# Performance work log

Hardware: AMD Instinct MI355X
Metric: run time of the kernel (lower is better)

The kernel has to match this reference:

```python
import jax, jax.numpy as jnp
import numpy as np

B, C, COUT, HEADS = 1, 256, 256, 8
H, W, KS = 96, 96, 7  # spatial dims and neighborhood kernel size


def _nbr_1d(n, k):
    # NATTEN/flex-mask style clamped window: center = clip(q, wl, n-1-wr)
    wl = k // 2
    wr = k // 2 + (k % 2 - 1)
    q = np.arange(n)
    center = np.clip(q, wl, n - 1 - wr)
    start = center - wl  # in [0, n-k]; window always fully in-bounds
    return start[:, None] + np.arange(k)[None, :]  # [n, k]


def _nbr_idx(h, w, k):
    ih = _nbr_1d(h, k)  # [h, k]
    iw = _nbr_1d(w, k)  # [w, k]
    flat = ih[:, None, :, None] * w + iw[None, :, None, :]  # [h, w, k, k]
    return jnp.asarray(flat.reshape(h * w, k * k))  # [S, K]


def setup_inputs() -> dict:
    key = jax.random.key(0)
    ks = jax.random.split(key, 4)
    x = jax.random.normal(ks[0], (B, C, H, W), jnp.float32)
    w_qkv = jax.random.normal(ks[1], (3 * C, C), jnp.float32) * (C ** -0.5)
    b_qkv = jnp.zeros((3 * C,), jnp.float32)
    w_out = jax.random.normal(ks[2], (COUT, C), jnp.float32) * (C ** -0.5)
    b_out = jnp.zeros((COUT,), jnp.float32)
    return {"x": x, "w_qkv": w_qkv, "b_qkv": b_qkv, "w_out": w_out, "b_out": b_out}


def reference(x, w_qkv, b_qkv, w_out, b_out):
    dh = C // HEADS
    S = H * W
    xl = jnp.moveaxis(x, 1, -1)  # [B,H,W,C]
    qkv = xl @ w_qkv.T + b_qkv  # [B,H,W,3C], layout (qkv, heads, dh) on last axis
    qkv = qkv.reshape(B, S, 3, HEADS, dh)
    q = jnp.transpose(qkv[:, :, 0], (0, 2, 1, 3))  # [B,heads,S,dh]
    k = jnp.transpose(qkv[:, :, 1], (0, 2, 1, 3))
    v = jnp.transpose(qkv[:, :, 2], (0, 2, 1, 3))
    # rope_embed_fraction = 0.0 -> RoPE is identity
    nbr = _nbr_idx(H, W, KS)  # [S, K] static neighbor indices, K = KS*KS
    k_nb = jnp.take(k, nbr, axis=2)  # [B,heads,S,K,dh]
    v_nb = jnp.take(v, nbr, axis=2)  # [B,heads,S,K,dh]
    scores = jnp.einsum('bhsd,bhskd->bhsk', q, k_nb) * (dh ** -0.5)
    attn = jax.nn.softmax(scores, axis=-1)  # window fully in-bounds -> no mask
    out = jnp.einsum('bhsk,bhskd->bhsd', attn, v_nb)  # [B,heads,S,dh]
    out = jnp.transpose(out, (0, 2, 1, 3)).reshape(B, S, HEADS * dh)
    out = out @ w_out.T + b_out  # [B,S,COUT]
    out = out.reshape(B, H, W, COUT)
    return jnp.moveaxis(out, -1, 1)  # [B,COUT,H,W]
```

## Files before the change

kernel.cpp:

```cpp
#include <hip/hip_runtime.h>
#include <hip/hip_bf16.h>
#include <math.h>

#define SD 9216
#define HH 96
#define CC 256
#define NO 768
#define NH 8
#define DH 32
#define NW1 (NO * CC)
#define NWT (NW1 + CC * CC)
#define PROW 232

typedef short bf16x8 __attribute__((ext_vector_type(8)));
typedef short short8v __attribute__((ext_vector_type(8)));
typedef float f32x4 __attribute__((ext_vector_type(4)));
typedef unsigned short us8 __attribute__((ext_vector_type(8)));

__device__ __forceinline__ float bf2f(unsigned short u) {
  union { unsigned u; float f; } c; c.u = ((unsigned)u) << 16; return c.f;
}
__device__ __forceinline__ unsigned short f2bf(float f) {
  unsigned u = __float_as_uint(f);
  unsigned r = (u + 0x7FFF + ((u >> 16) & 1)) >> 16;
  return (unsigned short)r;
}
__device__ __forceinline__ void gll16(const unsigned short* g, short* l) {
  __builtin_amdgcn_global_load_lds(
      (const __attribute__((address_space(1))) void*)g,
      (__attribute__((address_space(3))) void*)l, 16, 0, 0);
}

__global__ __launch_bounds__(256) void prep(const float* __restrict__ x,
                                            const float* __restrict__ wq,
                                            const float* __restrict__ wo,
                                            unsigned short* __restrict__ xbt,
                                            unsigned short* __restrict__ wdst) {
  __shared__ float tile[32][33];
  const int b = blockIdx.x;
  const int t = threadIdx.x;
  if (b < 2304) {
    const int s0 = (b % 288) * 32;
    const int c0 = (b / 288) * 32;
    {
      const int c = t >> 3, s4 = (t & 7) * 4;
      const float4 v = *(const float4*)(x + (size_t)(c0 + c) * SD + s0 + s4);
      tile[c][s4] = v.x; tile[c][s4 + 1] = v.y; tile[c][s4 + 2] = v.z; tile[c][s4 + 3] = v.w;
    }
    __syncthreads();
    {
      const int s = t >> 3, c4 = (t & 7) * 4;
      ushort4 o;
      o.x = f2bf(tile[c4][s]);     o.y = f2bf(tile[c4 + 1][s]);
      o.z = f2bf(tile[c4 + 2][s]); o.w = f2bf(tile[c4 + 3][s]);
      *(ushort4*)(xbt + (size_t)(s0 + s) * CC + c0 + c4) = o;
    }
  } else {
    const int i = ((b - 2304) * 256 + t) * 4;
    if (i < NWT) {
      const float* src = (i < NW1) ? (wq + i) : (wo + (i - NW1));
      const float4 v = *(const float4*)src;
      ushort4 o;
      o.x = f2bf(v.x); o.y = f2bf(v.y); o.z = f2bf(v.z); o.w = f2bf(v.w);
      *(ushort4*)(wdst + i) = o;
    }
  }
}

template <int BM, int BN, int EPI>
__global__ __launch_bounds__(256) void gemm_gll(const unsigned short* __restrict__ A,
                                                const unsigned short* __restrict__ Bm,
                                                const float* __restrict__ bias,
                                                void* __restrict__ out) {
  constexpr int MI = BM / 32, NJ = BN / 32;
  constexpr int STAGE_SH = (BM + BN) * 64;
  constexpr int CT_SH = (EPI == 0) ? BM * (BN + 8) : 2 * BM * (BN + 4);
  constexpr int SMEM_SH = STAGE_SH > CT_SH ? STAGE_SH : CT_SH;
  __shared__ __align__(16) short smem[SMEM_SH];
  short* Asd = smem;
  short* Bsd = smem + BM * 64;
  const int t = threadIdx.x;
  const int lane = t & 63;
  const int w = t >> 6;
  const int m0 = blockIdx.x * BM;
  const int n0 = blockIdx.y * BN;
  const int wm = (w >> 1) * (BM / 2);
  const int wn = (w & 1) * (BN / 2);
  f32x4 acc[MI][NJ] = {};
  const int l8 = lane >> 3;
  const int sl = lane & 7;

  for (int k0 = 0; k0 < CC; k0 += 64) {
#pragma unroll
    for (int q = 0; q < BM / 32; ++q) {
      const int r = w * (BM / 4) + q * 8 + l8;
      const int cs = sl ^ (r & 7);
      gll16(A + (size_t)(m0 + r) * CC + k0 + cs * 8, Asd + (w * (BM / 4) + q * 8) * 64);
    }
#pragma unroll
    for (int q = 0; q < BN / 32; ++q) {
      const int r = w * (BN / 4) + q * 8 + l8;
      const int cs = sl ^ (r & 7);
      gll16(Bm + (size_t)(n0 + r) * CC + k0 + cs * 8, Bsd + (w * (BN / 4) + q * 8) * 64);
    }
    __syncthreads();
    const int lr = lane & 15, g = lane >> 4;
#pragma unroll
    for (int kk = 0; kk < 2; ++kk) {
      bf16x8 af[MI], bf[NJ];
#pragma unroll
      for (int i = 0; i < MI; ++i) {
        const int row = wm + i * 16 + lr;
        af[i] = *(const bf16x8*)&Asd[row * 64 + ((kk * 4 + g) ^ (lr & 7)) * 8];
      }
#pragma unroll
      for (int j = 0; j < NJ; ++j) {
        const int row = wn + j * 16 + lr;
        bf[j] = *(const bf16x8*)&Bsd[row * 64 + ((kk * 4 + g) ^ (lr & 7)) * 8];
      }
#pragma unroll
      for (int i = 0; i < MI; ++i)
#pragma unroll
        for (int j = 0; j < NJ; ++j)
          acc[i][j] = __builtin_amdgcn_mfma_f32_16x16x32_bf16(af[i], bf[j], acc[i][j], 0, 0, 0);
    }
    __syncthreads();
  }

  const int lc = lane & 15, lr4 = (lane >> 4) * 4;
  if (EPI == 0) {
    unsigned short* O = (unsigned short*)out;
    unsigned short* Ct = (unsigned short*)smem;
#pragma unroll
    for (int i = 0; i < MI; ++i)
#pragma unroll
      for (int j = 0; j < NJ; ++j) {
        const float bb = bias[n0 + wn + j * 16 + lc];
#pragma unroll
        for (int r = 0; r < 4; ++r)
          Ct[(wm + i * 16 + lr4 + r) * (BN + 8) + wn + j * 16 + lc] = f2bf(acc[i][j][r] + bb);
      }
    __syncthreads();
#pragma unroll
    for (int rep = 0; rep < BM * BN / 8 / 256; ++rep) {
      const int c = rep * 256 + t;
      const int lrow = c / (BN / 8), lcol8 = (c % (BN / 8)) * 8;
      *(us8*)(O + (size_t)(m0 + lrow) * NO + n0 + lcol8) =
          *(const us8*)&Ct[lrow * (BN + 8) + lcol8];
    }
  } else {
    float* O = (float*)out;
    float* Cf = (float*)smem;
#pragma unroll
    for (int i = 0; i < MI; ++i)
#pragma unroll
      for (int j = 0; j < NJ; ++j) {
#pragma unroll
        for (int r = 0; r < 4; ++r) {
          const int lrow = wm + i * 16 + lr4 + r;
          Cf[lrow * (BN + 4) + wn + j * 16 + lc] = acc[i][j][r] + bias[m0 + lrow];
        }
      }
    __syncthreads();
#pragma unroll
    for (int rep = 0; rep < BM * BN / 4 / 256; ++rep) {
      const int c = rep * 256 + t;
      const int lrow = c / (BN / 4), lcol4 = (c % (BN / 4)) * 4;
      *(float4*)(O + (size_t)(m0 + lrow) * SD + n0 + lcol4) =
          *(const float4*)&Cf[lrow * (BN + 4) + lcol4];
    }
  }
}

__global__ __launch_bounds__(256) void nattn_mfma(const unsigned short* __restrict__ qkv,
                                                  unsigned short* __restrict__ att) {
  __shared__ int offs[224];
  __shared__ short Vt[32][PROW];
  __shared__ short Ps[4][16][PROW];
  const int t = threadIdx.x;
  const int lane = t & 63;
  const int w = t >> 6;
  const int g = lane >> 4;
  const int qcol = lane & 15;
  const int tile = blockIdx.x;
  const int h = blockIdx.y;
  const int ti = tile / 12, tj = tile % 12;
  const int qi0 = ti * 8, qj0 = tj * 8;
  const int ri0 = min(max(qi0, 3), 92) - 3;
  const int cj0 = min(max(qj0, 3), 92) - 3;

  if (t < 224) {
    const int kr = min(t, 195);
    const int ru = kr / 14, cu = kr - ru * 14;
    offs[t] = (min(ri0 + ru, 95) * HH + min(cj0 + cu, 95)) * NO;
  }

  const int ql = w * 16 + qcol;
  const int qi = qi0 + (ql >> 3), qj = qj0 + (ql & 7);
  const int dr = min(max(qi, 3), 92) - 3 - ri0;
  const int dc = min(max(qj, 3), 92) - 3 - cj0;
  const bf16x8 qf = *(const bf16x8*)(qkv + (size_t)(qi * HH + qj) * NO + h * DH + g * 8);
  __syncthreads();

  us8 vreg[4];
  const int kg4 = t >> 2, d0 = (t & 3) * 8;
  if (t < 224) {
#pragma unroll
    for (int kk = 0; kk < 4; ++kk)
      vreg[kk] = *(const us8*)(qkv + (size_t)offs[kg4 * 4 + kk] + 2 * CC + h * DH + d0);
  }

  f32x4 c[13];
#pragma unroll
  for (int m = 0; m < 13; ++m) {
    const bf16x8 kf = *(const bf16x8*)(qkv + (size_t)offs[16 * m + qcol] + CC + h * DH + g * 8);
    c[m] = __builtin_amdgcn_mfma_f32_16x16x32_bf16(kf, qf, (f32x4){0.f, 0.f, 0.f, 0.f}, 0, 0, 0);
  }

  float mx = -1e30f;
#pragma unroll
  for (int m = 0; m < 13; ++m)
#pragma unroll
    for (int r = 0; r < 4; ++r) {
      const int ku = 16 * m + 4 * g + r;
      const unsigned ru = (unsigned)ku / 14u, cu = (unsigned)ku % 14u;
      const bool ok = (ku < 196) && ((unsigned)((int)ru - dr) <= 6u) && ((unsigned)((int)cu - dc) <= 6u);
      const float s = ok ? c[m][r] * 0.17677669529663687f : -1e30f;
      c[m][r] = s;
      mx = fmaxf(mx, s);
    }
  mx = fmaxf(mx, __shfl_xor(mx, 16));
  mx = fmaxf(mx, __shfl_xor(mx, 32));
  float sum = 0.f;
#pragma unroll
  for (int m = 0; m < 13; ++m)
#pragma unroll
    for (int r = 0; r < 4; ++r) { const float p = __expf(c[m][r] - mx); c[m][r] = p; sum += p; }
  sum += __shfl_xor(sum, 16);
  sum += __shfl_xor(sum, 32);
  const float inv = 1.0f / sum;

#pragma unroll
  for (int m = 0; m < 13; ++m) {
    ushort4 pk;
    pk.x = f2bf(c[m][0] * inv); pk.y = f2bf(c[m][1] * inv);
    pk.z = f2bf(c[m][2] * inv); pk.w = f2bf(c[m][3] * inv);
    *(ushort4*)&Ps[w][qcol][16 * m + 4 * g] = pk;
  }
  if (lane < 32) {
    const short8v z = {0, 0, 0, 0, 0, 0, 0, 0};
    *(short8v*)&Ps[w][lane >> 1][208 + (lane & 1) * 8] = z;
  }

  if (t < 224) {
#pragma unroll
    for (int jj = 0; jj < 8; ++jj) {
      ushort4 o;
      o.x = vreg[0][jj]; o.y = vreg[1][jj]; o.z = vreg[2][jj]; o.w = vreg[3][jj];
      *(ushort4*)&Vt[d0 + jj][kg4 * 4] = o;
    }
  }
  __syncthreads();

  f32x4 o0 = {0.f, 0.f, 0.f, 0.f}, o1 = {0.f, 0.f, 0.f, 0.f};
#pragma unroll
  for (int tt = 0; tt < 7; ++tt) {
    const bf16x8 pa = *(const bf16x8*)&Ps[w][qcol][tt * 32 + g * 8];
    const bf16x8 v0 = *(const bf16x8*)&Vt[qcol][tt * 32 + g * 8];
    const bf16x8 v1 = *(const bf16x8*)&Vt[16 + qcol][tt * 32 + g * 8];
    o0 = __builtin_amdgcn_mfma_f32_16x16x32_bf16(pa, v0, o0, 0, 0, 0);
    o1 = __builtin_amdgcn_mfma_f32_16x16x32_bf16(pa, v1, o1, 0, 0, 0);
  }

#pragma unroll
  for (int r = 0; r < 4; ++r) {
    const int qlr = w * 16 + g * 4 + r;
    const int s = (qi0 + (qlr >> 3)) * HH + qj0 + (qlr & 7);
    unsigned short* ap = att + (size_t)s * CC + h * DH;
    ap[qcol] = f2bf(o0[r]);
    ap[16 + qcol] = f2bf(o1[r]);
  }
}

extern "C" void kernel_launch(void* const* d_in, const int* in_sizes, int n_in,
                              void* d_out, int out_size, void* d_ws, size_t ws_size,
                              hipStream_t stream) {
  const float* x     = (const float*)d_in[0];
  const float* w_qkv = (const float*)d_in[1];
  const float* b_qkv = (const float*)d_in[2];
  const float* w_out = (const float*)d_in[3];
  const float* b_out = (const float*)d_in[4];
  float* out = (float*)d_out;

  unsigned short* ws   = (unsigned short*)d_ws;
  unsigned short* xbt  = ws;
  unsigned short* wqb  = xbt + (size_t)SD * CC;
  unsigned short* wob  = wqb + (size_t)NO * CC;
  unsigned short* qkvb = wob + (size_t)CC * CC;
  unsigned short* attb = qkvb + (size_t)SD * NO;

  prep<<<dim3(2304 + NWT / 4 / 256), dim3(256), 0, stream>>>(x, w_qkv, w_out, xbt, wqb);

  gemm_gll<128, 128, 0><<<dim3(SD / 128, NO / 128), dim3(256), 0, stream>>>(xbt, wqb, b_qkv, qkvb);

  nattn_mfma<<<dim3(144, NH), dim3(256), 0, stream>>>(qkvb, attb);

  gemm_gll<64, 128, 1><<<dim3(CC / 64, SD / 128), dim3(256), 0, stream>>>(wob, attb, b_out, out);
}
```

Measured before the change: 105.7 us.

## Pad neighborhood rows to 16, bitmask validity, shrink P staging, retile QKV GEMM

Result: faster. 101.8 us (-3.7%).

```diff
diff --git a/kernel.cpp b/kernel.cpp
--- a/kernel.cpp
+++ b/kernel.cpp
@@ -13,13 +13,9 @@
 #define PROW 232
 
 typedef short bf16x8 __attribute__((ext_vector_type(8)));
-typedef short short8v __attribute__((ext_vector_type(8)));
 typedef float f32x4 __attribute__((ext_vector_type(4)));
 typedef unsigned short us8 __attribute__((ext_vector_type(8)));
 
-__device__ __forceinline__ float bf2f(unsigned short u) {
-  union { unsigned u; float f; } c; c.u = ((unsigned)u) << 16; return c.f;
-}
 __device__ __forceinline__ unsigned short f2bf(float f) {
   unsigned u = __float_as_uint(f);
   unsigned r = (u + 0x7FFF + ((u >> 16) & 1)) >> 16;
@@ -176,7 +172,7 @@
                                                   unsigned short* __restrict__ att) {
   __shared__ int offs[224];
   __shared__ short Vt[32][PROW];
-  __shared__ short Ps[4][16][PROW];
+  __shared__ unsigned Pst[4][16][20];
   const int t = threadIdx.x;
   const int lane = t & 63;
   const int w = t >> 6;
@@ -190,8 +186,7 @@
   const int cj0 = min(max(qj0, 3), 92) - 3;
 
   if (t < 224) {
-    const int kr = min(t, 195);
-    const int ru = kr / 14, cu = kr - ru * 14;
+    const int ru = t >> 4, cu = min(t & 15, 13);
     offs[t] = (min(ri0 + ru, 95) * HH + min(cj0 + cu, 95)) * NO;
   }
 
@@ -199,6 +194,8 @@
   const int qi = qi0 + (ql >> 3), qj = qj0 + (ql & 7);
   const int dr = min(max(qi, 3), 92) - 3 - ri0;
   const int dc = min(max(qj, 3), 92) - 3 - cj0;
+  const unsigned rowmask = 0x7Fu << dr;
+  const unsigned colm4 = (0x7Fu << dc) >> (4 * g);
   const bf16x8 qf = *(const bf16x8*)(qkv + (size_t)(qi * HH + qj) * NO + h * DH + g * 8);
   __syncthreads();
 
@@ -210,21 +207,19 @@
       vreg[kk] = *(const us8*)(qkv + (size_t)offs[kg4 * 4 + kk] + 2 * CC + h * DH + d0);
   }
 
-  f32x4 c[13];
-#pragma unroll
-  for (int m = 0; m < 13; ++m) {
+  f32x4 c[14];
+#pragma unroll
+  for (int m = 0; m < 14; ++m) {
     const bf16x8 kf = *(const bf16x8*)(qkv + (size_t)offs[16 * m + qcol] + CC + h * DH + g * 8);
     c[m] = __builtin_amdgcn_mfma_f32_16x16x32_bf16(kf, qf, (f32x4){0.f, 0.f, 0.f, 0.f}, 0, 0, 0);
   }
 
   float mx = -1e30f;
 #pragma unroll
-  for (int m = 0; m < 13; ++m)
+  for (int m = 0; m < 14; ++m)
 #pragma unroll
     for (int r = 0; r < 4; ++r) {
-      const int ku = 16 * m + 4 * g + r;
-      const unsigned ru = (unsigned)ku / 14u, cu = (unsigned)ku % 14u;
-      const bool ok = (ku < 196) && ((unsigned)((int)ru - dr) <= 6u) && ((unsigned)((int)cu - dc) <= 6u);
+      const bool ok = ((rowmask >> m) & 1u) && ((colm4 >> r) & 1u);
       const float s = ok ? c[m][r] * 0.17677669529663687f : -1e30f;
       c[m][r] = s;
       mx = fmaxf(mx, s);
@@ -233,23 +228,18 @@
   mx = fmaxf(mx, __shfl_xor(mx, 32));
   float sum = 0.f;
 #pragma unroll
-  for (int m = 0; m < 13; ++m)
+  for (int m = 0; m < 14; ++m)
 #pragma unroll
     for (int r = 0; r < 4; ++r) { const float p = __expf(c[m][r] - mx); c[m][r] = p; sum += p; }
   sum += __shfl_xor(sum, 16);
   sum += __shfl_xor(sum, 32);
   const float inv = 1.0f / sum;
 
-#pragma unroll
-  for (int m = 0; m < 13; ++m) {
-    ushort4 pk;
-    pk.x = f2bf(c[m][0] * inv); pk.y = f2bf(c[m][1] * inv);
-    pk.z = f2bf(c[m][2] * inv); pk.w = f2bf(c[m][3] * inv);
-    *(ushort4*)&Ps[w][qcol][16 * m + 4 * g] = pk;
-  }
-  if (lane < 32) {
-    const short8v z = {0, 0, 0, 0, 0, 0, 0, 0};
-    *(short8v*)&Ps[w][lane >> 1][208 + (lane & 1) * 8] = z;
+  unsigned pk[14][2];
+#pragma unroll
+  for (int m = 0; m < 14; ++m) {
+    pk[m][0] = (unsigned)f2bf(c[m][0] * inv) | ((unsigned)f2bf(c[m][1] * inv) << 16);
+    pk[m][1] = (unsigned)f2bf(c[m][2] * inv) | ((unsigned)f2bf(c[m][3] * inv) << 16);
   }
 
   if (t < 224) {
@@ -265,7 +255,9 @@
   f32x4 o0 = {0.f, 0.f, 0.f, 0.f}, o1 = {0.f, 0.f, 0.f, 0.f};
 #pragma unroll
   for (int tt = 0; tt < 7; ++tt) {
-    const bf16x8 pa = *(const bf16x8*)&Ps[w][qcol][tt * 32 + g * 8];
+    *(uint2*)&Pst[w][qcol][2 * g] = make_uint2(pk[2 * tt][0], pk[2 * tt][1]);
+    *(uint2*)&Pst[w][qcol][8 + 2 * g] = make_uint2(pk[2 * tt + 1][0], pk[2 * tt + 1][1]);
+    const bf16x8 pa = *(const bf16x8*)&Pst[w][qcol][4 * g];
     const bf16x8 v0 = *(const bf16x8*)&Vt[qcol][tt * 32 + g * 8];
     const bf16x8 v1 = *(const bf16x8*)&Vt[16 + qcol][tt * 32 + g * 8];
     o0 = __builtin_amdgcn_mfma_f32_16x16x32_bf16(pa, v0, o0, 0, 0, 0);
@@ -301,7 +293,7 @@
 
   prep<<<dim3(2304 + NWT / 4 / 256), dim3(256), 0, stream>>>(x, w_qkv, w_out, xbt, wqb);
 
-  gemm_gll<128, 128, 0><<<dim3(SD / 128, NO / 128), dim3(256), 0, stream>>>(xbt, wqb, b_qkv, qkvb);
+  gemm_gll<64, 128, 0><<<dim3(SD / 64, NO / 128), dim3(256), 0, stream>>>(xbt, wqb, b_qkv, qkvb);
 
   nattn_mfma<<<dim3(144, NH), dim3(256), 0, stream>>>(qkvb, attb);
 
```
